# Kernel tuning notes

Measured on AMD Instinct MI355X. Metric: run time of the kernel, lower is better.

The kernel has to match this reference:

```python
import jax, jax.numpy as jnp
import numpy as np

B, C_IN, C_OUT, N, K = 4, 384, 768, 8192, 16
GROUPS = 4


def setup_inputs() -> dict:
    key = jax.random.key(0)
    k1, k2, k3 = jax.random.split(key, 3)
    x = jax.random.normal(k1, (B, C_IN, N, 1), dtype=jnp.float32)
    edge_index = jax.random.randint(k2, (2, B, N, K), 0, N)
    # grouped 1x1 conv weight: [C_OUT, (2*C_IN)//GROUPS] (kaiming-normal-like init)
    fan_in = 2 * C_IN // GROUPS
    W = jax.random.normal(k3, (C_OUT, fan_in), dtype=jnp.float32) * np.float32((2.0 / fan_in) ** 0.5)
    b = jnp.zeros((C_OUT,), jnp.float32)
    return {"x": x, "edge_index": edge_index, "W": W, "b": b}


def reference(x, edge_index, W, b):
    # x: [B, C, N, 1]; edge_index: [2, B, N, K]
    x3 = x[..., 0]  # [B, C, N]
    gather = jax.vmap(lambda f, i: f[:, i])  # f:[C,N], i:[N,K] -> [C,N,K]
    x_i = gather(x3, edge_index[1])  # [B, C, N, K]
    x_j = gather(x3, edge_index[0])  # [B, C, N, K]
    rel = jnp.max(x_j - x_i, axis=-1)  # [B, C, N]  (max-relative aggregation)
    # torch: cat([x.unsqueeze(2), rel.unsqueeze(2)], dim=2).reshape(b, 2c, n, 1)
    # -> channels interleaved (x_c, rel_c) pairs
    merged = jnp.stack([x3, rel], axis=2).reshape(B, 2 * C_IN, N)
    # grouped 1x1 conv (groups=4)
    cin_g = 2 * C_IN // GROUPS
    cout_g = C_OUT // GROUPS
    xg = merged.reshape(B, GROUPS, cin_g, N)
    Wg = W.reshape(GROUPS, cout_g, cin_g)
    out = jnp.einsum("bgin,goi->bgon", xg, Wg).reshape(B, C_OUT, N, 1)
    out = out + b[None, :, None, None]
    return jax.nn.relu(out)
```

## Files before the change

### kernel.cpp

```cpp
#include <hip/hip_runtime.h>
#include <hip/hip_bf16.h>

#define B_ 4
#define C_IN_ 384
#define C_OUT_ 768
#define N_ 8192
#define K_ 16
#define FANIN_ 192
#define NT 32
#define PADC (2*C_IN_ + 8)

typedef float f32x4 __attribute__((ext_vector_type(4)));
typedef short bf16x8 __attribute__((ext_vector_type(8)));

__device__ __forceinline__ unsigned short f2b(float f) {
  union { float f; unsigned u; } v; v.f = f;
  unsigned r = v.u + 0x7FFFu + ((v.u >> 16) & 1u);
  return (unsigned short)(r >> 16);
}

__global__ __launch_bounds__(256) void wconv_kernel(const float* __restrict__ W,
                                                    unsigned short* __restrict__ Wb) {
  int i = blockIdx.x * 256 + threadIdx.x;
  if (i < C_OUT_ * FANIN_) Wb[i] = f2b(W[i]);
}

__global__ __launch_bounds__(256) void transpose_kernel(const float* __restrict__ x,
                                                        unsigned short* __restrict__ xt,
                                                        char* __restrict__ xq) {
  __shared__ float tile[32][65];
  int n0 = blockIdx.x * 32;
  int c0 = blockIdx.y * 64;
  int b  = blockIdx.z;
  int tx = threadIdx.x & 31;
  int ty = threadIdx.x >> 5;
  const float* xp = x + (size_t)b * C_IN_ * N_;
  #pragma unroll
  for (int r = 0; r < 8; ++r) {
    int c = c0 + r * 8 + ty;
    tile[tx][r * 8 + ty] = xp[(size_t)c * N_ + n0 + tx];
  }
  __syncthreads();
  unsigned short* outp = xt + ((size_t)b * N_ + n0) * C_IN_ + c0;
  int cp = threadIdx.x & 31;
  int ny = threadIdx.x >> 5;
  #pragma unroll
  for (int p = 0; p < 4; ++p) {
    int nl = ny + p * 8;
    unsigned pk = (unsigned)f2b(tile[nl][cp * 2]) |
                  ((unsigned)f2b(tile[nl][cp * 2 + 1]) << 16);
    *(unsigned*)(outp + (size_t)nl * C_IN_ + cp * 2) = pk;
  }
  char* qout = xq + ((size_t)b * N_ + n0) * C_IN_ + c0;
  #pragma unroll
  for (int u = 0; u < 2; ++u) {
    int uu = u * 256 + threadIdx.x;
    int nl = uu >> 4;
    int c4 = uu & 15;
    unsigned pk = 0;
    #pragma unroll
    for (int e = 0; e < 4; ++e) {
      int q = __float2int_rn(tile[nl][c4 * 4 + e] * 16.0f);
      q = q > 127 ? 127 : (q < -127 ? -127 : q);
      pk |= ((unsigned)(q & 0xff)) << (8 * e);
    }
    *(unsigned*)(qout + (size_t)nl * C_IN_ + c4 * 4) = pk;
  }
}

__global__ __launch_bounds__(512) void mrconv_kernel(
    const unsigned short* __restrict__ xt,
    const char* __restrict__ xq,
    const int* __restrict__ eidx,
    const unsigned short* __restrict__ Wb,
    const float* __restrict__ bias,
    float* __restrict__ out)
{
  __shared__ unsigned short m_lds[NT][PADC];
  int tile = blockIdx.x;
  int b    = blockIdx.y;
  int n0   = tile * NT;
  int tid  = threadIdx.x;
  int wv   = tid >> 6;
  int lane = tid & 63;

  const unsigned short* xtb = xt + (size_t)b * N_ * C_IN_;
  const char* xqb = xq + (size_t)b * N_ * C_IN_;
  const int* e0p = eidx + ((size_t)b * N_) * K_;
  const int* e1p = eidx + ((size_t)(B_ + b) * N_) * K_;

  for (int s = 0; s < 4; ++s) {
    int nl = wv * 4 + s;
    int nb = __builtin_amdgcn_readfirstlane(n0 + nl);
    const int* e0 = e0p + (size_t)nb * K_;
    const int* e1 = e1p + (size_t)nb * K_;
    if (lane < 48) {
      uint4 xv = *(const uint4*)(xtb + (size_t)nb * C_IN_ + lane * 8);
      const char* xqc = xqb + lane * 8;

      uint2 vj[K_], vi[K_];
      #pragma unroll
      for (int k = 0; k < K_; ++k) {
        int j = __builtin_amdgcn_readfirstlane(e0[k]);
        vj[k] = *(const uint2*)(xqc + (size_t)j * C_IN_);
      }
      #pragma unroll
      for (int k = 0; k < K_; ++k) {
        int i = __builtin_amdgcn_readfirstlane(e1[k]);
        vi[k] = *(const uint2*)(xqc + (size_t)i * C_IN_);
      }

      int mx[8];
      #pragma unroll
      for (int c = 0; c < 8; ++c) mx[c] = -512;
      #pragma unroll
      for (int k = 0; k < K_; ++k) {
        unsigned aj[2] = {vj[k].x, vj[k].y};
        unsigned ai[2] = {vi[k].x, vi[k].y};
        #pragma unroll
        for (int d = 0; d < 2; ++d)
          #pragma unroll
          for (int e = 0; e < 4; ++e) {
            int sj = (int)(signed char)((aj[d] >> (8 * e)) & 0xffu);
            int si = (int)(signed char)((ai[d] >> (8 * e)) & 0xffu);
            int df = sj - si;
            mx[4 * d + e] = df > mx[4 * d + e] ? df : mx[4 * d + e];
          }
      }

      unsigned ux[4] = {xv.x, xv.y, xv.z, xv.w};
      unsigned od[8];
      #pragma unroll
      for (int c = 0; c < 8; ++c) {
        unsigned xs = (ux[c >> 1] >> ((c & 1) * 16)) & 0xffffu;
        od[c] = xs | ((unsigned)f2b((float)mx[c] * 0.0625f) << 16);
      }
      uint4 o0; o0.x = od[0]; o0.y = od[1]; o0.z = od[2]; o0.w = od[3];
      uint4 o1; o1.x = od[4]; o1.y = od[5]; o1.z = od[6]; o1.w = od[7];
      *(uint4*)&m_lds[nl][lane * 16] = o0;
      *(uint4*)&m_lds[nl][lane * 16 + 8] = o1;
    }
  }
  __syncthreads();

  int g    = wv >> 1;
  int half = wv & 1;
  int rb   = g * 192 + half * 96;
  int l15  = lane & 15;
  int lhi  = lane >> 4;

  f32x4 acc[6][2];
  #pragma unroll
  for (int rt = 0; rt < 6; ++rt)
    #pragma unroll
    for (int ct = 0; ct < 2; ++ct)
      acc[rt][ct] = (f32x4){0.f, 0.f, 0.f, 0.f};

  #pragma unroll
  for (int ks = 0; ks < 6; ++ks) {
    int k0 = ks * 32 + lhi * 8;
    bf16x8 bfrag[2];
    #pragma unroll
    for (int ct = 0; ct < 2; ++ct) {
      int n = ct * 16 + l15;
      bfrag[ct] = *(const bf16x8*)&m_lds[n][g * FANIN_ + k0];
    }
    #pragma unroll
    for (int rt = 0; rt < 6; ++rt) {
      int co = rb + rt * 16 + l15;
      bf16x8 afrag = *(const bf16x8*)(Wb + (size_t)co * FANIN_ + k0);
      #pragma unroll
      for (int ct = 0; ct < 2; ++ct)
        acc[rt][ct] = __builtin_amdgcn_mfma_f32_16x16x32_bf16(afrag, bfrag[ct],
                                                              acc[rt][ct], 0, 0, 0);
    }
  }

  float* outb = out + (size_t)b * C_OUT_ * N_;
  #pragma unroll
  for (int rt = 0; rt < 6; ++rt) {
    int co_b = rb + rt * 16 + lhi * 4;
    #pragma unroll
    for (int ct = 0; ct < 2; ++ct) {
      int n = n0 + ct * 16 + l15;
      #pragma unroll
      for (int r = 0; r < 4; ++r) {
        int co = co_b + r;
        float v = acc[rt][ct][r] + bias[co];
        outb[(size_t)co * N_ + n] = v > 0.f ? v : 0.f;
      }
    }
  }
}

extern "C" void kernel_launch(void* const* d_in, const int* in_sizes, int n_in,
                              void* d_out, int out_size, void* d_ws, size_t ws_size,
                              hipStream_t stream) {
  const float* x    = (const float*)d_in[0];
  const int*   eidx = (const int*)d_in[1];
  const float* W    = (const float*)d_in[2];
  const float* bias = (const float*)d_in[3];
  float* out = (float*)d_out;

  unsigned short* xt = (unsigned short*)d_ws;
  unsigned short* Wb = xt + (size_t)B_ * N_ * C_IN_;
  char*           xq = (char*)(Wb + (size_t)C_OUT_ * FANIN_);

  wconv_kernel<<<(C_OUT_ * FANIN_ + 255) / 256, 256, 0, stream>>>(W, Wb);

  dim3 tg(N_ / 32, C_IN_ / 64, B_);
  transpose_kernel<<<tg, 256, 0, stream>>>(x, xt, xq);

  dim3 mg(N_ / NT, B_);
  mrconv_kernel<<<mg, 512, 0, stream>>>(xt, xq, eidx, Wb, bias, out);
}
```

Measured before the change: 103.5 us.

## Split K across wave halves, use packed 16-bit max on offset-binary int8 gather

The gather stage now uses all 64 lanes: each half-wave handles alternate neighbors over 12 channels per lane, and the two halves are combined with a cross-half shuffle max. Int8 values are stored offset-binary (unsigned + 128) so even and odd bytes can be unpacked with masks into packed 16-bit lanes, and the max-relative reduction runs as packed subtract and max. The merged LDS tile is de-interleaved (x channels first, then rel channels per group), and W columns are permuted to match, which avoids interleaving work in the producer. This is meant to cut idle lanes and per-byte ALU work in the gather phase, at the cost of more shuffles and a more complex index mapping.

Result: faster. 94.97 us (-8.3%).

```diff
diff --git a/kernel.cpp b/kernel.cpp
--- a/kernel.cpp
+++ b/kernel.cpp
@@ -12,6 +12,7 @@
 
 typedef float f32x4 __attribute__((ext_vector_type(4)));
 typedef short bf16x8 __attribute__((ext_vector_type(8)));
+typedef short s16x2 __attribute__((ext_vector_type(2)));
 
 __device__ __forceinline__ unsigned short f2b(float f) {
   union { float f; unsigned u; } v; v.f = f;
@@ -22,12 +23,17 @@
 __global__ __launch_bounds__(256) void wconv_kernel(const float* __restrict__ W,
                                                     unsigned short* __restrict__ Wb) {
   int i = blockIdx.x * 256 + threadIdx.x;
-  if (i < C_OUT_ * FANIN_) Wb[i] = f2b(W[i]);
+  if (i < C_OUT_ * FANIN_) {
+    int kp = i % FANIN_;
+    int o  = i / FANIN_;
+    int f  = (kp < 96) ? (2 * kp) : (2 * (kp - 96) + 1);
+    Wb[i] = f2b(W[(size_t)o * FANIN_ + f]);
+  }
 }
 
 __global__ __launch_bounds__(256) void transpose_kernel(const float* __restrict__ x,
                                                         unsigned short* __restrict__ xt,
-                                                        char* __restrict__ xq) {
+                                                        unsigned char* __restrict__ xq) {
   __shared__ float tile[32][65];
   int n0 = blockIdx.x * 32;
   int c0 = blockIdx.y * 64;
@@ -51,7 +57,7 @@
                   ((unsigned)f2b(tile[nl][cp * 2 + 1]) << 16);
     *(unsigned*)(outp + (size_t)nl * C_IN_ + cp * 2) = pk;
   }
-  char* qout = xq + ((size_t)b * N_ + n0) * C_IN_ + c0;
+  unsigned char* qout = xq + ((size_t)b * N_ + n0) * C_IN_ + c0;
   #pragma unroll
   for (int u = 0; u < 2; ++u) {
     int uu = u * 256 + threadIdx.x;
@@ -60,9 +66,9 @@
     unsigned pk = 0;
     #pragma unroll
     for (int e = 0; e < 4; ++e) {
-      int q = __float2int_rn(tile[nl][c4 * 4 + e] * 16.0f);
-      q = q > 127 ? 127 : (q < -127 ? -127 : q);
-      pk |= ((unsigned)(q & 0xff)) << (8 * e);
+      int q = __float2int_rn(tile[nl][c4 * 4 + e] * 16.0f) + 128;
+      q = q < 0 ? 0 : (q > 255 ? 255 : q);
+      pk |= ((unsigned)q) << (8 * e);
     }
     *(unsigned*)(qout + (size_t)nl * C_IN_ + c4 * 4) = pk;
   }
@@ -70,7 +76,7 @@
 
 __global__ __launch_bounds__(512) void mrconv_kernel(
     const unsigned short* __restrict__ xt,
-    const char* __restrict__ xq,
+    const unsigned char* __restrict__ xq,
     const int* __restrict__ eidx,
     const unsigned short* __restrict__ Wb,
     const float* __restrict__ bias,
@@ -83,69 +89,97 @@
   int tid  = threadIdx.x;
   int wv   = tid >> 6;
   int lane = tid & 63;
+  int h    = lane >> 5;
+  int c    = lane & 31;
 
   const unsigned short* xtb = xt + (size_t)b * N_ * C_IN_;
-  const char* xqb = xq + (size_t)b * N_ * C_IN_;
+  const unsigned char*  xqb = xq + (size_t)b * N_ * C_IN_;
   const int* e0p = eidx + ((size_t)b * N_) * K_;
   const int* e1p = eidx + ((size_t)(B_ + b) * N_) * K_;
+
+  const unsigned char* xqc = xqb + c * 12;
 
   for (int s = 0; s < 4; ++s) {
     int nl = wv * 4 + s;
     int nb = __builtin_amdgcn_readfirstlane(n0 + nl);
     const int* e0 = e0p + (size_t)nb * K_;
     const int* e1 = e1p + (size_t)nb * K_;
+    int sj[16], si[16];
+    #pragma unroll
+    for (int k = 0; k < 16; ++k) {
+      sj[k] = __builtin_amdgcn_readfirstlane(e0[k]);
+      si[k] = __builtin_amdgcn_readfirstlane(e1[k]);
+    }
+    uint4 xv;
+    if (lane < 48) xv = *(const uint4*)(xtb + (size_t)nb * C_IN_ + lane * 8);
+
+    s16x2 me[3], mo[3];
+    #pragma unroll
+    for (int d = 0; d < 3; ++d) {
+      me[d] = (s16x2){-512, -512};
+      mo[d] = (s16x2){-512, -512};
+    }
+
+    #pragma unroll
+    for (int t = 0; t < 8; ++t) {
+      int jrow = h ? sj[2 * t + 1] : sj[2 * t];
+      int irow = h ? si[2 * t + 1] : si[2 * t];
+      uint3 vj = *(const uint3*)(xqc + (size_t)jrow * C_IN_);
+      uint3 vi = *(const uint3*)(xqc + (size_t)irow * C_IN_);
+      unsigned uj[3] = {vj.x, vj.y, vj.z};
+      unsigned ui[3] = {vi.x, vi.y, vi.z};
+      #pragma unroll
+      for (int d = 0; d < 3; ++d) {
+        s16x2 je = __builtin_bit_cast(s16x2, uj[d] & 0x00FF00FFu);
+        s16x2 jo = __builtin_bit_cast(s16x2, (uj[d] >> 8) & 0x00FF00FFu);
+        s16x2 ie = __builtin_bit_cast(s16x2, ui[d] & 0x00FF00FFu);
+        s16x2 io = __builtin_bit_cast(s16x2, (ui[d] >> 8) & 0x00FF00FFu);
+        s16x2 de = je - ie;
+        s16x2 dd = jo - io;
+        me[d] = __builtin_elementwise_max(me[d], de);
+        mo[d] = __builtin_elementwise_max(mo[d], dd);
+      }
+    }
+    #pragma unroll
+    for (int d = 0; d < 3; ++d) {
+      s16x2 oe = __builtin_bit_cast(s16x2, __shfl_xor(__builtin_bit_cast(int, me[d]), 32));
+      me[d] = __builtin_elementwise_max(me[d], oe);
+      s16x2 oo = __builtin_bit_cast(s16x2, __shfl_xor(__builtin_bit_cast(int, mo[d]), 32));
+      mo[d] = __builtin_elementwise_max(mo[d], oo);
+    }
+
+    int col = nl;
+    if (h == 0) {
+      int gch = c * 12;
+      int g   = gch / 96;
+      int pos = g * 192 + 96 + (gch - g * 96);
+      unsigned short* dst = &m_lds[col][pos];
+      unsigned w[6];
+      #pragma unroll
+      for (int d = 0; d < 3; ++d) {
+        unsigned w0 = f2b((float)me[d][0] * 0.0625f);
+        unsigned w1 = f2b((float)mo[d][0] * 0.0625f);
+        unsigned w2 = f2b((float)me[d][1] * 0.0625f);
+        unsigned w3 = f2b((float)mo[d][1] * 0.0625f);
+        w[2 * d]     = w0 | (w1 << 16);
+        w[2 * d + 1] = w2 | (w3 << 16);
+      }
+      *(uint2*)(dst)     = (uint2){w[0], w[1]};
+      *(uint2*)(dst + 4) = (uint2){w[2], w[3]};
+      *(uint2*)(dst + 8) = (uint2){w[4], w[5]};
+    }
     if (lane < 48) {
-      uint4 xv = *(const uint4*)(xtb + (size_t)nb * C_IN_ + lane * 8);
-      const char* xqc = xqb + lane * 8;
-
-      uint2 vj[K_], vi[K_];
-      #pragma unroll
-      for (int k = 0; k < K_; ++k) {
-        int j = __builtin_amdgcn_readfirstlane(e0[k]);
-        vj[k] = *(const uint2*)(xqc + (size_t)j * C_IN_);
-      }
-      #pragma unroll
-      for (int k = 0; k < K_; ++k) {
-        int i = __builtin_amdgcn_readfirstlane(e1[k]);
-        vi[k] = *(const uint2*)(xqc + (size_t)i * C_IN_);
-      }
-
-      int mx[8];
-      #pragma unroll
-      for (int c = 0; c < 8; ++c) mx[c] = -512;
-      #pragma unroll
-      for (int k = 0; k < K_; ++k) {
-        unsigned aj[2] = {vj[k].x, vj[k].y};
-        unsigned ai[2] = {vi[k].x, vi[k].y};
-        #pragma unroll
-        for (int d = 0; d < 2; ++d)
-          #pragma unroll
-          for (int e = 0; e < 4; ++e) {
-            int sj = (int)(signed char)((aj[d] >> (8 * e)) & 0xffu);
-            int si = (int)(signed char)((ai[d] >> (8 * e)) & 0xffu);
-            int df = sj - si;
-            mx[4 * d + e] = df > mx[4 * d + e] ? df : mx[4 * d + e];
-          }
-      }
-
-      unsigned ux[4] = {xv.x, xv.y, xv.z, xv.w};
-      unsigned od[8];
-      #pragma unroll
-      for (int c = 0; c < 8; ++c) {
-        unsigned xs = (ux[c >> 1] >> ((c & 1) * 16)) & 0xffffu;
-        od[c] = xs | ((unsigned)f2b((float)mx[c] * 0.0625f) << 16);
-      }
-      uint4 o0; o0.x = od[0]; o0.y = od[1]; o0.z = od[2]; o0.w = od[3];
-      uint4 o1; o1.x = od[4]; o1.y = od[5]; o1.z = od[6]; o1.w = od[7];
-      *(uint4*)&m_lds[nl][lane * 16] = o0;
-      *(uint4*)&m_lds[nl][lane * 16 + 8] = o1;
+      int gch = lane * 8;
+      int g   = gch / 96;
+      int pos = g * 192 + (gch - g * 96);
+      *(uint4*)&m_lds[col][pos] = xv;
     }
   }
   __syncthreads();
 
-  int g    = wv >> 1;
+  int g2   = wv >> 1;
   int half = wv & 1;
-  int rb   = g * 192 + half * 96;
+  int rb   = g2 * 192 + half * 96;
   int l15  = lane & 15;
   int lhi  = lane >> 4;
 
@@ -163,7 +197,7 @@
     #pragma unroll
     for (int ct = 0; ct < 2; ++ct) {
       int n = ct * 16 + l15;
-      bfrag[ct] = *(const bf16x8*)&m_lds[n][g * FANIN_ + k0];
+      bfrag[ct] = *(const bf16x8*)&m_lds[n][g2 * 192 + k0];
     }
     #pragma unroll
     for (int rt = 0; rt < 6; ++rt) {
@@ -204,7 +238,7 @@
 
   unsigned short* xt = (unsigned short*)d_ws;
   unsigned short* Wb = xt + (size_t)B_ * N_ * C_IN_;
-  char*           xq = (char*)(Wb + (size_t)C_OUT_ * FANIN_);
+  unsigned char*  xq = (unsigned char*)(Wb + (size_t)C_OUT_ * FANIN_);
 
   wconv_kernel<<<(C_OUT_ * FANIN_ + 255) / 256, 256, 0, stream>>>(W, Wb);
 
```
